# Optimization experiments

Measured on AMD Instinct MI355X. Metric: run time of the kernel, lower is better.

The kernel has to match this reference:

```python
import jax, jax.numpy as jnp
import numpy as np

N = 10000      # nodes
E = 320000     # edges (before self-loops)
IN = 128       # input features
HID = 32       # hidden channels per head
HEADS = 8
OUT = 40       # classes
NEG_SLOPE = 0.2  # PyG GATConv leaky_relu slope


def gat_conv(x, W, a_src, a_dst, b, src, dst, n, concat):
    """One PyG-style GATConv (eval mode, self-loops already in src/dst)."""
    H, C = a_src.shape
    xp = (x @ W).reshape(n, H, C)                       # [N,H,C]
    al_s = jnp.einsum('nhc,hc->nh', xp, a_src)          # [N,H]
    al_d = jnp.einsum('nhc,hc->nh', xp, a_dst)          # [N,H]
    e = jax.nn.leaky_relu(al_s[src] + al_d[dst], NEG_SLOPE)  # [E,H]
    # segment softmax over incoming edges of each dst node
    m = jax.ops.segment_max(e, dst, num_segments=n)
    ee = jnp.exp(e - m[dst])
    s = jax.ops.segment_sum(ee, dst, num_segments=n)
    alpha = ee / (s[dst] + 1e-16)                       # [E,H]
    out = jax.ops.segment_sum(alpha[:, :, None] * xp[src], dst, num_segments=n)  # [N,H,C]
    out = out.reshape(n, H * C) if concat else out.mean(axis=1)
    return out + b


def setup_inputs() -> dict:
    key = jax.random.key(0)
    ks = jax.random.split(key, 16)
    p = lambda k, shape: (jax.random.normal(k, shape, jnp.float32) * 0.1)
    HC = HEADS * HID
    return {
        'x': jax.random.normal(ks[0], (N, IN), jnp.float32),
        'edge_index': jax.random.randint(ks[1], (2, E), 0, N),
        'W1': p(ks[2], (IN, HC)), 'a_src1': p(ks[3], (HEADS, HID)), 'a_dst1': p(ks[4], (HEADS, HID)), 'b1': jnp.zeros((HC,), jnp.float32),
        'W2': p(ks[5], (HC, HC)), 'a_src2': p(ks[6], (HEADS, HID)), 'a_dst2': p(ks[7], (HEADS, HID)), 'b2': jnp.zeros((HC,), jnp.float32),
        'W3': p(ks[8], (HC, OUT)), 'a_src3': p(ks[9], (1, OUT)), 'a_dst3': p(ks[10], (1, OUT)), 'b3': jnp.zeros((OUT,), jnp.float32),
    }


def reference(x, edge_index, W1, a_src1, a_dst1, b1, W2, a_src2, a_dst2, b2,
              W3, a_src3, a_dst3, b3):
    n = x.shape[0]
    loop = jnp.arange(n, dtype=edge_index.dtype)
    src = jnp.concatenate([edge_index[0], loop])   # PyG add_self_loops=True
    dst = jnp.concatenate([edge_index[1], loop])
    h = jax.nn.elu(gat_conv(x, W1, a_src1, a_dst1, b1, src, dst, n, True))
    h = jax.nn.elu(gat_conv(h, W2, a_src2, a_dst2, b2, src, dst, n, True))
    h = gat_conv(h, W3, a_src3, a_dst3, b3, src, dst, n, False)
    return jax.nn.log_softmax(h, axis=1)
```

## Files before the change

### kernel.cpp

```cpp
#include <hip/hip_runtime.h>
#include <hip/hip_bf16.h>
#include <math.h>


#define DEV_INLINE __device__ __forceinline__

typedef __attribute__((ext_vector_type(8))) short short8;
typedef __attribute__((ext_vector_type(4))) float f32x4;
typedef __attribute__((ext_vector_type(2))) float f32x2;
typedef unsigned short ushort_t;
typedef unsigned int uint_t;
typedef unsigned char uchar_t;

#define ELLW 128

#if defined(__has_builtin)
#if __has_builtin(__builtin_amdgcn_cvt_pk_f32_fp8) && __has_builtin(__builtin_amdgcn_cvt_pk_fp8_f32)
#define FP8_HW 1
#endif
#endif
#ifndef FP8_HW
#define FP8_HW 0
#endif

DEV_INLINE float leaky02(float x) { return x > 0.f ? x : 0.2f * x; }
DEV_INLINE float elu1(float x) { return x > 0.f ? x : expm1f(x); }

DEV_INLINE ushort_t f2bf(float f) {
    uint_t u = __float_as_uint(f);
    u += 0x7FFFu + ((u >> 16) & 1u);
    return (ushort_t)(u >> 16);
}
DEV_INLINE float bf2f(ushort_t u) { return __uint_as_float(((uint_t)u) << 16); }


DEV_INLINE uint_t f2fp8(float v) {
#if FP8_HW
    return __builtin_amdgcn_cvt_pk_fp8_f32(v, v, 0, false) & 0xFFu;
#else
    float a = fabsf(v);
    uint_t s = (__float_as_uint(v) >> 24) & 0x80u;
    if (!(a >= 0.0009765625f)) return s;
    if (a >= 448.f) return s | 0x7Eu;
    if (a < 0.015625f) {
        int m = (int)(a * 512.f + 0.5f);
        if (m >= 8) return s | 0x08u;
        return s | (uint_t)m;
    }
    uint_t ab = __float_as_uint(a);
    uint_t r = ab + 0x0007FFFFu + ((ab >> 20) & 1u);
    uint_t e = (r >> 23) - 127u + 7u;
    uint_t m = (r >> 20) & 7u;
    if (e > 15u || (e == 15u && m == 7u)) return s | 0x7Eu;
    return s | (e << 3) | m;
#endif
}

DEV_INLINE void fp8x8_dec(uint2 w, float* f) {
#if FP8_HW
    f32x2 a0 = __builtin_amdgcn_cvt_pk_f32_fp8((int)w.x, false);
    f32x2 a1 = __builtin_amdgcn_cvt_pk_f32_fp8((int)w.x, true);
    f32x2 a2 = __builtin_amdgcn_cvt_pk_f32_fp8((int)w.y, false);
    f32x2 a3 = __builtin_amdgcn_cvt_pk_f32_fp8((int)w.y, true);
    f[0] = a0.x; f[1] = a0.y; f[2] = a1.x; f[3] = a1.y;
    f[4] = a2.x; f[5] = a2.y; f[6] = a3.x; f[7] = a3.y;
#else
    uint_t b[8] = {w.x & 255u, (w.x >> 8) & 255u, (w.x >> 16) & 255u, w.x >> 24,
                   w.y & 255u, (w.y >> 8) & 255u, (w.y >> 16) & 255u, w.y >> 24};
#pragma unroll
    for (int i = 0; i < 8; ++i) {
        uint_t em = b[i] & 0x7Fu;
        float mag = (em >= 8u) ? __uint_as_float(0x3C000000u + (em << 20))
                               : (float)(int)em * 0.001953125f;
        f[i] = (b[i] & 0x80u) ? -mag : mag;
    }
#endif
}


__global__ void prep_kernel(const float* __restrict__ W1, ushort_t* __restrict__ W1T,
                            const float* __restrict__ W2, ushort_t* __restrict__ W2T,
                            const float* __restrict__ W3, ushort_t* __restrict__ W3T,
                            const float* __restrict__ as1, const float* __restrict__ ad1,
                            const float* __restrict__ as2, const float* __restrict__ ad2,
                            const float* __restrict__ as3, const float* __restrict__ ad3,
                            int* __restrict__ cursor, int n) {
    int i = blockIdx.x * blockDim.x + threadIdx.x;
    if (i < n) { cursor[i] = 0; return; }
    i -= n;
    if (i < 128 * 256) {
        int k = i >> 8, c = i & 255;
        W1T[(size_t)c * 128 + k] = f2bf(W1[i]);
        return;
    }
    i -= 128 * 256;
    if (i < 256 * 256) {
        int k = i >> 8, c = i & 255;
        W2T[(size_t)c * 256 + k] = f2bf(W2[i]);
        return;
    }
    i -= 256 * 256;
    if (i < 256 * 40) {
        int k = i / 40, c = i - k * 40;
        W3T[(size_t)c * 256 + k] = f2bf(W3[i]);
        return;
    }
    i -= 256 * 40;
    if (i < 1024) {
        int h = i >> 7, k = i & 127;
        float acc = 0.f;
#pragma unroll
        for (int c = 0; c < 32; ++c) acc += W1[k * 256 + h * 32 + c] * as1[h * 32 + c];
        W1T[(size_t)(256 + h) * 128 + k] = f2bf(acc);
        return;
    }
    i -= 1024;
    if (i < 1024) {
        int h = i >> 7, k = i & 127;
        float acc = 0.f;
#pragma unroll
        for (int c = 0; c < 32; ++c) acc += W1[k * 256 + h * 32 + c] * ad1[h * 32 + c];
        W1T[(size_t)(264 + h) * 128 + k] = f2bf(acc);
        return;
    }
    i -= 1024;
    if (i < 2048) {
        int h = i >> 8, k = i & 255;
        float acc = 0.f;
#pragma unroll
        for (int c = 0; c < 32; ++c) acc += W2[k * 256 + h * 32 + c] * as2[h * 32 + c];
        W2T[(size_t)(256 + h) * 256 + k] = f2bf(acc);
        return;
    }
    i -= 2048;
    if (i < 2048) {
        int h = i >> 8, k = i & 255;
        float acc = 0.f;
#pragma unroll
        for (int c = 0; c < 32; ++c) acc += W2[k * 256 + h * 32 + c] * ad2[h * 32 + c];
        W2T[(size_t)(264 + h) * 256 + k] = f2bf(acc);
        return;
    }
    i -= 2048;
    if (i < 256) {
        float acc = 0.f;
#pragma unroll
        for (int c = 0; c < 40; ++c) acc += W3[i * 40 + c] * as3[c];
        W3T[(size_t)40 * 256 + i] = f2bf(acc);
        return;
    }
    i -= 256;
    if (i < 256) {
        float acc = 0.f;
#pragma unroll
        for (int c = 0; c < 40; ++c) acc += W3[i * 40 + c] * ad3[c];
        W3T[(size_t)41 * 256 + i] = f2bf(acc);
        return;
    }
}


DEV_INLINE int lds_slot(int r, int c) { return r * 4 + ((c + (r >> 1)) & 3); }

DEV_INLINE void gemm_body(ushort_t* __restrict__ As, ushort_t* __restrict__ Bs,
                          const ushort_t* __restrict__ A, const ushort_t* __restrict__ BT,
                          uchar_t* __restrict__ C8,
                          float* __restrict__ ALS, float* __restrict__ ALD,
                          int M, int NOUT, int NH, int NTOT, int K, int bx, int by) {
    const int tid = threadIdx.x;
    const int wave = tid >> 6, lane = tid & 63;
    const int row0 = by * 64;
    const int col0 = bx * 64;

    const int sr = tid >> 2, sc = tid & 3;
    const int a_row = row0 + sr;
    const int b_row = col0 + sr;

    const int fr = lane & 15;
    const int fc = lane >> 4;

    f32x4 acc0 = {}, acc1 = {}, acc2 = {}, acc3 = {};

    for (int k0 = 0; k0 < K; k0 += 32) {
        short8 av = {}, bv = {};
        if (a_row < M) av = *(const short8*)(A + (size_t)a_row * K + k0 + sc * 8);
        if (b_row < NTOT) bv = *(const short8*)(BT + (size_t)b_row * K + k0 + sc * 8);
        __syncthreads();
        *(short8*)(As + lds_slot(sr, sc) * 8) = av;
        *(short8*)(Bs + lds_slot(sr, sc) * 8) = bv;
        __syncthreads();

        const int arow = wave * 16 + fr;
        short8 afrag = *(const short8*)(As + lds_slot(arow, fc) * 8);
        short8 b0 = *(const short8*)(Bs + lds_slot(0 * 16 + fr, fc) * 8);
        short8 b1 = *(const short8*)(Bs + lds_slot(1 * 16 + fr, fc) * 8);
        short8 b2 = *(const short8*)(Bs + lds_slot(2 * 16 + fr, fc) * 8);
        short8 b3 = *(const short8*)(Bs + lds_slot(3 * 16 + fr, fc) * 8);
        acc0 = __builtin_amdgcn_mfma_f32_16x16x32_bf16(afrag, b0, acc0, 0, 0, 0);
        acc1 = __builtin_amdgcn_mfma_f32_16x16x32_bf16(afrag, b1, acc1, 0, 0, 0);
        acc2 = __builtin_amdgcn_mfma_f32_16x16x32_bf16(afrag, b2, acc2, 0, 0, 0);
        acc3 = __builtin_amdgcn_mfma_f32_16x16x32_bf16(afrag, b3, acc3, 0, 0, 0);
    }
    __syncthreads();

    const int crow = row0 + wave * 16 + (lane >> 4) * 4;
    const int ccol = col0 + (lane & 15);
    f32x4 accs[4] = {acc0, acc1, acc2, acc3};
#pragma unroll
    for (int ct = 0; ct < 4; ++ct) {
        int col = ccol + ct * 16;
#pragma unroll
        for (int j = 0; j < 4; ++j) {
            int row = crow + j;
            if (row >= M) continue;
            float v = accs[ct][j];
            if (col < NOUT) {
                C8[(size_t)row * NOUT + col] = (uchar_t)f2fp8(v);
            } else {
                int cc = col - NOUT;
                if (cc < NH) ALS[(size_t)row * NH + cc] = v;
                else if (cc < 2 * NH) ALD[(size_t)row * NH + (cc - NH)] = v;
            }
        }
    }
}

DEV_INLINE void gemm1_body(ushort_t* __restrict__ As, ushort_t* __restrict__ Bs,
                           const float* __restrict__ X, const ushort_t* __restrict__ BT,
                           uchar_t* __restrict__ C8, float* __restrict__ ALS,
                           float* __restrict__ ALD, int M, int bx, int by) {
    const int tid = threadIdx.x;
    const int wave = tid >> 6, lane = tid & 63;
    const int row0 = by * 64;
    const int col0 = bx * 64;

    const int sr = tid >> 2, sc = tid & 3;
    const int a_row = row0 + sr;
    const int b_row = col0 + sr;

    const int fr = lane & 15;
    const int fc = lane >> 4;

    f32x4 acc0 = {}, acc1 = {}, acc2 = {}, acc3 = {};

    for (int k0 = 0; k0 < 128; k0 += 32) {
        short8 av = {}, bv = {};
        if (a_row < M) {
            const float* xp = X + (size_t)a_row * 128 + k0 + sc * 8;
            float4 f0 = *(const float4*)(xp);
            float4 f1 = *(const float4*)(xp + 4);
            av[0] = (short)f2bf(f0.x); av[1] = (short)f2bf(f0.y);
            av[2] = (short)f2bf(f0.z); av[3] = (short)f2bf(f0.w);
            av[4] = (short)f2bf(f1.x); av[5] = (short)f2bf(f1.y);
            av[6] = (short)f2bf(f1.z); av[7] = (short)f2bf(f1.w);
        }
        if (b_row < 272) bv = *(const short8*)(BT + (size_t)b_row * 128 + k0 + sc * 8);
        __syncthreads();
        *(short8*)(As + lds_slot(sr, sc) * 8) = av;
        *(short8*)(Bs + lds_slot(sr, sc) * 8) = bv;
        __syncthreads();

        const int arow = wave * 16 + fr;
        short8 afrag = *(const short8*)(As + lds_slot(arow, fc) * 8);
        short8 b0 = *(const short8*)(Bs + lds_slot(0 * 16 + fr, fc) * 8);
        short8 b1 = *(const short8*)(Bs + lds_slot(1 * 16 + fr, fc) * 8);
        short8 b2 = *(const short8*)(Bs + lds_slot(2 * 16 + fr, fc) * 8);
        short8 b3 = *(const short8*)(Bs + lds_slot(3 * 16 + fr, fc) * 8);
        acc0 = __builtin_amdgcn_mfma_f32_16x16x32_bf16(afrag, b0, acc0, 0, 0, 0);
        acc1 = __builtin_amdgcn_mfma_f32_16x16x32_bf16(afrag, b1, acc1, 0, 0, 0);
        acc2 = __builtin_amdgcn_mfma_f32_16x16x32_bf16(afrag, b2, acc2, 0, 0, 0);
        acc3 = __builtin_amdgcn_mfma_f32_16x16x32_bf16(afrag, b3, acc3, 0, 0, 0);
    }
    __syncthreads();

    const int crow = row0 + wave * 16 + (lane >> 4) * 4;
    const int ccol = col0 + (lane & 15);
    f32x4 accs[4] = {acc0, acc1, acc2, acc3};
#pragma unroll
    for (int ct = 0; ct < 4; ++ct) {
        int col = ccol + ct * 16;
#pragma unroll
        for (int j = 0; j < 4; ++j) {
            int row = crow + j;
            if (row >= M) continue;
            float v = accs[ct][j];
            if (col < 256) {
                C8[(size_t)row * 256 + col] = (uchar_t)f2fp8(v);
            } else {
                int cc = col - 256;
                if (cc < 8) ALS[(size_t)row * 8 + cc] = v;
                else if (cc < 16) ALD[(size_t)row * 8 + (cc - 8)] = v;
            }
        }
    }
}

__global__ __launch_bounds__(256) void gemm_kernel(const ushort_t* __restrict__ A,
                                                   const ushort_t* __restrict__ BT,
                                                   uchar_t* __restrict__ C8,
                                                   float* __restrict__ ALS,
                                                   float* __restrict__ ALD,
                                                   int M, int NOUT, int NH, int NTOT,
                                                   int K, int gx) {
    __shared__ ushort_t As[64 * 32];
    __shared__ ushort_t Bs[64 * 32];
    gemm_body(As, Bs, A, BT, C8, ALS, ALD, M, NOUT, NH, NTOT, K,
              blockIdx.x % gx, blockIdx.x / gx);
}

__global__ __launch_bounds__(256) void scatter_gemm1_kernel(const int* __restrict__ src,
                                                            const int* __restrict__ dst,
                                                            int* __restrict__ cursor,
                                                            int* __restrict__ ell, int e,
                                                            int svb,
                                                            const float* __restrict__ X,
                                                            const ushort_t* __restrict__ BT,
                                                            uchar_t* __restrict__ C8,
                                                            float* __restrict__ ALS,
                                                            float* __restrict__ ALD,
                                                            int M, int gx) {
    __shared__ ushort_t As[64 * 32];
    __shared__ ushort_t Bs[64 * 32];
    if (blockIdx.x < svb) {
        int i = blockIdx.x * 256 + threadIdx.x;
        if (i < e) {
            int d = dst[i];
            int p = atomicAdd(&cursor[d], 1);
            ell[d * ELLW + p] = src[i];
        }
        return;
    }
    int b = blockIdx.x - svb;
    gemm1_body(As, Bs, X, BT, C8, ALS, ALD, M, b % gx, b / gx);
}


template <int FUSE3>
__global__ __launch_bounds__(256) void aggregate_h8_kernel(const uchar_t* __restrict__ xp8,
                                                           const float* __restrict__ als,
                                                           const float* __restrict__ ald,
                                                           const int* __restrict__ degv,
                                                           const int* __restrict__ ell,
                                                           const float* __restrict__ bias,
                                                           ushort_t* __restrict__ out,
                                                           const ushort_t* __restrict__ W3T,
                                                           ushort_t* __restrict__ xp3,
                                                           float* __restrict__ als3,
                                                           float* __restrict__ ald3,
                                                           int n) {
    int node = (blockIdx.x * blockDim.x + threadIdx.x) >> 6;
    int lane = threadIdx.x & 63;
    if (node >= n) return;
    const int half = lane >> 5;
    const int lh = lane & 31;
    const int ch = lh * 8;
    const int head = lh >> 2;
    const int deg = degv[node];
    const int rs = node * ELLW, re = rs + deg;
    const float ad = ald[node * 8 + head];
    const float m = leaky02(als[node * 8 + head] + ad);

    float acc[8];
    float ssum;
    if (half == 0) {
        uint2 sv = *(const uint2*)(xp8 + (size_t)node * 256 + ch);
        float sf[8];
        fp8x8_dec(sv, sf);
#pragma unroll
        for (int i = 0; i < 8; ++i) acc[i] = sf[i];
        ssum = 1.0f;
    } else {
#pragma unroll
        for (int i = 0; i < 8; ++i) acc[i] = 0.f;
        ssum = 0.f;
    }

    for (int base = rs; base < re; base += 64) {
        const int cnt = (re - base < 64) ? (re - base) : 64;
        int myi = (lane < cnt) ? ell[base + lane] : 0;
        int j = 0;
        for (; j + 8 <= cnt; j += 8) {
            int s0 = __shfl(myi, j + half);
            int s1 = __shfl(myi, j + 2 + half);
            int s2 = __shfl(myi, j + 4 + half);
            int s3 = __shfl(myi, j + 6 + half);
            float a0 = als[s0 * 8 + head];
            float a1 = als[s1 * 8 + head];
            float a2 = als[s2 * 8 + head];
            float a3 = als[s3 * 8 + head];
            uint2 v0 = *(const uint2*)(xp8 + (size_t)s0 * 256 + ch);
            uint2 v1 = *(const uint2*)(xp8 + (size_t)s1 * 256 + ch);
            uint2 v2 = *(const uint2*)(xp8 + (size_t)s2 * 256 + ch);
            uint2 v3 = *(const uint2*)(xp8 + (size_t)s3 * 256 + ch);
            float p0 = __expf(leaky02(a0 + ad) - m);
            float p1 = __expf(leaky02(a1 + ad) - m);
            float p2 = __expf(leaky02(a2 + ad) - m);
            float p3 = __expf(leaky02(a3 + ad) - m);
            ssum += (p0 + p1) + (p2 + p3);
            float f0[8], f1[8], f2[8], f3[8];
            fp8x8_dec(v0, f0);
            fp8x8_dec(v1, f1);
            fp8x8_dec(v2, f2);
            fp8x8_dec(v3, f3);
#pragma unroll
            for (int i = 0; i < 8; ++i)
                acc[i] += (p0 * f0[i] + p1 * f1[i]) + (p2 * f2[i] + p3 * f3[i]);
        }
        for (; j < cnt; j += 2) {
            int jj = j + half;
            int s = __shfl(myi, jj & 63);
            bool valid = jj < cnt;
            float a = als[s * 8 + head];
            uint2 v = *(const uint2*)(xp8 + (size_t)s * 256 + ch);
            float p = valid ? __expf(leaky02(a + ad) - m) : 0.f;
            ssum += p;
            float fv[8];
            fp8x8_dec(v, fv);
#pragma unroll
            for (int i = 0; i < 8; ++i) acc[i] += p * fv[i];
        }
    }

    ssum += __shfl_xor(ssum, 32);
#pragma unroll
    for (int i = 0; i < 8; ++i) acc[i] += __shfl_xor(acc[i], 32);

    if (FUSE3 == 0) {
        if (half == 0) {
            float inv = 1.f / ssum;
            float4 ba = *(const float4*)(bias + ch);
            float4 bb = *(const float4*)(bias + ch + 4);
            float bv[8] = {ba.x, ba.y, ba.z, ba.w, bb.x, bb.y, bb.z, bb.w};
            short8 o;
#pragma unroll
            for (int i = 0; i < 8; ++i) o[i] = (short)f2bf(elu1(acc[i] * inv + bv[i]));
            *(short8*)(out + (size_t)node * 256 + ch) = o;
        }
    } else {
        float inv = 1.f / ssum;
        float4 ba = *(const float4*)(bias + ch);
        float4 bb = *(const float4*)(bias + ch + 4);
        float bv[8] = {ba.x, ba.y, ba.z, ba.w, bb.x, bb.y, bb.z, bb.w};
        float hf[8];
#pragma unroll
        for (int i = 0; i < 8; ++i) hf[i] = elu1(acc[i] * inv + bv[i]);

        float res = 0.f;
#pragma unroll
        for (int idx = 0; idx < 21; ++idx) {
            int c = half * 21 + idx;
            short8 w = *(const short8*)(W3T + (size_t)c * 256 + ch);
            float p = hf[0] * bf2f((ushort_t)w[0]) + hf[1] * bf2f((ushort_t)w[1])
                    + hf[2] * bf2f((ushort_t)w[2]) + hf[3] * bf2f((ushort_t)w[3])
                    + hf[4] * bf2f((ushort_t)w[4]) + hf[5] * bf2f((ushort_t)w[5])
                    + hf[6] * bf2f((ushort_t)w[6]) + hf[7] * bf2f((ushort_t)w[7]);
            p += __shfl_xor(p, 1);
            p += __shfl_xor(p, 2);
            p += __shfl_xor(p, 4);
            p += __shfl_xor(p, 8);
            p += __shfl_xor(p, 16);
            if (lh == idx) res = p;
        }
        if (lh < 21) {
            int c = half * 21 + lh;
            if (c < 40)      xp3[(size_t)node * 40 + c] = f2bf(res);
            else if (c == 40) als3[node] = res;
            else             ald3[node] = res;
        }
    }
}


__global__ __launch_bounds__(256) void aggregate_out_kernel(const ushort_t* __restrict__ xp,
                                                            const float* __restrict__ als,
                                                            const float* __restrict__ ald,
                                                            const int* __restrict__ degv,
                                                            const int* __restrict__ ell,
                                                            const float* __restrict__ bias,
                                                            float* __restrict__ out, int n) {
    int node = (blockIdx.x * blockDim.x + threadIdx.x) >> 6;
    int lane = threadIdx.x & 63;
    if (node >= n) return;
    const int half = lane >> 5;
    const int lh = lane & 31;
    const bool act = lh < 20;
    const int ch = lh * 2;
    const int deg = degv[node];
    const int rs = node * ELLW, re = rs + deg;
    const float ad = ald[node];
    const float m = leaky02(als[node] + ad);

    float a0, a1, ssum;
    if (half == 0) {
        if (act) {
            ushort2 sv = *(const ushort2*)(xp + (size_t)node * 40 + ch);
            a0 = bf2f(sv.x); a1 = bf2f(sv.y);
        } else { a0 = a1 = 0.f; }
        ssum = 1.0f;
    } else { a0 = a1 = 0.f; ssum = 0.f; }

    for (int base = rs; base < re; base += 64) {
        const int cnt = (re - base < 64) ? (re - base) : 64;
        int myi = (lane < cnt) ? ell[base + lane] : 0;
        int j = 0;
        for (; j + 8 <= cnt; j += 8) {
            int s0 = __shfl(myi, j + half);
            int s1 = __shfl(myi, j + 2 + half);
            int s2 = __shfl(myi, j + 4 + half);
            int s3 = __shfl(myi, j + 6 + half);
            float e0 = als[s0];
            float e1 = als[s1];
            float e2 = als[s2];
            float e3 = als[s3];
            ushort2 v0 = act ? *(const ushort2*)(xp + (size_t)s0 * 40 + ch) : ushort2{0, 0};
            ushort2 v1 = act ? *(const ushort2*)(xp + (size_t)s1 * 40 + ch) : ushort2{0, 0};
            ushort2 v2 = act ? *(const ushort2*)(xp + (size_t)s2 * 40 + ch) : ushort2{0, 0};
            ushort2 v3 = act ? *(const ushort2*)(xp + (size_t)s3 * 40 + ch) : ushort2{0, 0};
            float p0 = __expf(leaky02(e0 + ad) - m);
            float p1 = __expf(leaky02(e1 + ad) - m);
            float p2 = __expf(leaky02(e2 + ad) - m);
            float p3 = __expf(leaky02(e3 + ad) - m);
            ssum += (p0 + p1) + (p2 + p3);
            a0 += (p0 * bf2f(v0.x) + p1 * bf2f(v1.x)) + (p2 * bf2f(v2.x) + p3 * bf2f(v3.x));
            a1 += (p0 * bf2f(v0.y) + p1 * bf2f(v1.y)) + (p2 * bf2f(v2.y) + p3 * bf2f(v3.y));
        }
        for (; j < cnt; j += 2) {
            int jj = j + half;
            int s = __shfl(myi, jj & 63);
            bool valid = jj < cnt;
            float a = als[s];
            ushort2 v = act ? *(const ushort2*)(xp + (size_t)s * 40 + ch) : ushort2{0, 0};
            float p = valid ? __expf(leaky02(a + ad) - m) : 0.f;
            ssum += p;
            a0 += p * bf2f(v.x);
            a1 += p * bf2f(v.y);
        }
    }

    ssum += __shfl_xor(ssum, 32);
    a0 += __shfl_xor(a0, 32);
    a1 += __shfl_xor(a1, 32);

    float inv = 1.f / ssum;
    float2 b2 = act ? *(const float2*)(bias + ch) : float2{0.f, 0.f};
    float o0 = act ? (a0 * inv + b2.x) : -INFINITY;
    float o1 = act ? (a1 * inv + b2.y) : -INFINITY;

    float mx = fmaxf(o0, o1);
#pragma unroll
    for (int off = 16; off >= 1; off >>= 1) mx = fmaxf(mx, __shfl_xor(mx, off));
    float ex = act ? (__expf(o0 - mx) + __expf(o1 - mx)) : 0.f;
#pragma unroll
    for (int off = 16; off >= 1; off >>= 1) ex += __shfl_xor(ex, off);
    float lse = mx + __logf(ex);
    if (half == 0 && act) {
        float2 o = {o0 - lse, o1 - lse};
        *(float2*)(out + (size_t)node * 40 + ch) = o;
    }
}


extern "C" void kernel_launch(void* const* d_in, const int* in_sizes, int n_in,
                              void* d_out, int out_size, void* d_ws, size_t ws_size,
                              hipStream_t stream) {
    const float* x      = (const float*)d_in[0];
    const int*   edge   = (const int*)d_in[1];
    const float* W1     = (const float*)d_in[2];
    const float* a_src1 = (const float*)d_in[3];
    const float* a_dst1 = (const float*)d_in[4];
    const float* b1     = (const float*)d_in[5];
    const float* W2     = (const float*)d_in[6];
    const float* a_src2 = (const float*)d_in[7];
    const float* a_dst2 = (const float*)d_in[8];
    const float* b2     = (const float*)d_in[9];
    const float* W3     = (const float*)d_in[10];
    const float* a_src3 = (const float*)d_in[11];
    const float* a_dst3 = (const float*)d_in[12];
    const float* b3     = (const float*)d_in[13];
    float* out = (float*)d_out;

    const int n = in_sizes[0] / 128;
    const int e = in_sizes[1] / 2;

    char* ws = (char*)d_ws;
    size_t off = 0;
    auto alloc = [&](size_t bytes) -> void* {
        void* p = ws + off;
        off += (bytes + 255) & ~(size_t)255;
        return p;
    };
    uchar_t*  xp8       = (uchar_t*)alloc((size_t)n * 256);
    ushort_t* h_bf      = (ushort_t*)alloc((size_t)n * 256 * 2);
    ushort_t* xp3       = (ushort_t*)alloc((size_t)n * 40 * 2);
    ushort_t* W1T       = (ushort_t*)alloc((size_t)272 * 128 * 2);
    ushort_t* W2T       = (ushort_t*)alloc((size_t)272 * 256 * 2);
    ushort_t* W3T       = (ushort_t*)alloc((size_t)42 * 256 * 2);
    float*    als       = (float*)alloc((size_t)n * 8 * 4);
    float*    ald       = (float*)alloc((size_t)n * 8 * 4);
    float*    als3      = (float*)alloc((size_t)n * 4);
    float*    ald3      = (float*)alloc((size_t)n * 4);
    int*      cursor    = (int*)alloc((size_t)n * 4);
    int*      ell       = (int*)alloc((size_t)n * ELLW * 4);
    (void)ws_size;

    const int* srcs = edge;
    const int* dsts = edge + e;

    const int mby = (n + 63) / 64;
    const int svb = (e + 255) / 256;

    {
        int prep_total = n + 128 * 256 + 256 * 256 + 256 * 40
                       + 1024 + 1024 + 2048 + 2048 + 256 + 256;
        prep_kernel<<<(prep_total + 255) / 256, 256, 0, stream>>>(
            W1, W1T, W2, W2T, W3, W3T,
            a_src1, a_dst1, a_src2, a_dst2, a_src3, a_dst3, cursor, n);
    }
    scatter_gemm1_kernel<<<svb + 5 * mby, 256, 0, stream>>>(
        srcs, dsts, cursor, ell, e, svb, x, W1T, xp8, als, ald, n, 5);

    const int agg_grid = (n * 64 + 255) / 256;

    aggregate_h8_kernel<0><<<agg_grid, 256, 0, stream>>>(
        xp8, als, ald, cursor, ell, b1, h_bf, nullptr, nullptr, nullptr, nullptr, n);
    gemm_kernel<<<5 * mby, 256, 0, stream>>>(h_bf, W2T, xp8, als, ald,
                                             n, 256, 8, 272, 256, 5);
    aggregate_h8_kernel<1><<<agg_grid, 256, 0, stream>>>(
        xp8, als, ald, cursor, ell, b2, nullptr, W3T, xp3, als3, ald3, n);
    aggregate_out_kernel<<<agg_grid, 256, 0, stream>>>(xp3, als3, ald3, cursor, ell, b3, out, n);
}
```

Before: 101.5 us.

## Fuse attention logits into GEMM epilogue and fold weight prep into scatter kernel

```diff
diff --git a/kernel.cpp b/kernel.cpp
--- a/kernel.cpp
+++ b/kernel.cpp
@@ -78,22 +78,10 @@
 }
 
 
-__global__ void prep_kernel(const float* __restrict__ W1, ushort_t* __restrict__ W1T,
-                            const float* __restrict__ W2, ushort_t* __restrict__ W2T,
-                            const float* __restrict__ W3, ushort_t* __restrict__ W3T,
-                            const float* __restrict__ as1, const float* __restrict__ ad1,
-                            const float* __restrict__ as2, const float* __restrict__ ad2,
-                            const float* __restrict__ as3, const float* __restrict__ ad3,
-                            int* __restrict__ cursor, int n) {
-    int i = blockIdx.x * blockDim.x + threadIdx.x;
-    if (i < n) { cursor[i] = 0; return; }
-    i -= n;
-    if (i < 128 * 256) {
-        int k = i >> 8, c = i & 255;
-        W1T[(size_t)c * 128 + k] = f2bf(W1[i]);
-        return;
-    }
-    i -= 128 * 256;
+DEV_INLINE void prep_body(int i,
+                          const float* __restrict__ W2, ushort_t* __restrict__ W2T,
+                          const float* __restrict__ W3, ushort_t* __restrict__ W3T,
+                          const float* __restrict__ as3, const float* __restrict__ ad3) {
     if (i < 256 * 256) {
         int k = i >> 8, c = i & 255;
         W2T[(size_t)c * 256 + k] = f2bf(W2[i]);
@@ -106,42 +94,6 @@
         return;
     }
     i -= 256 * 40;
-    if (i < 1024) {
-        int h = i >> 7, k = i & 127;
-        float acc = 0.f;
-#pragma unroll
-        for (int c = 0; c < 32; ++c) acc += W1[k * 256 + h * 32 + c] * as1[h * 32 + c];
-        W1T[(size_t)(256 + h) * 128 + k] = f2bf(acc);
-        return;
-    }
-    i -= 1024;
-    if (i < 1024) {
-        int h = i >> 7, k = i & 127;
-        float acc = 0.f;
-#pragma unroll
-        for (int c = 0; c < 32; ++c) acc += W1[k * 256 + h * 32 + c] * ad1[h * 32 + c];
-        W1T[(size_t)(264 + h) * 128 + k] = f2bf(acc);
-        return;
-    }
-    i -= 1024;
-    if (i < 2048) {
-        int h = i >> 8, k = i & 255;
-        float acc = 0.f;
-#pragma unroll
-        for (int c = 0; c < 32; ++c) acc += W2[k * 256 + h * 32 + c] * as2[h * 32 + c];
-        W2T[(size_t)(256 + h) * 256 + k] = f2bf(acc);
-        return;
-    }
-    i -= 2048;
-    if (i < 2048) {
-        int h = i >> 8, k = i & 255;
-        float acc = 0.f;
-#pragma unroll
-        for (int c = 0; c < 32; ++c) acc += W2[k * 256 + h * 32 + c] * ad2[h * 32 + c];
-        W2T[(size_t)(264 + h) * 256 + k] = f2bf(acc);
-        return;
-    }
-    i -= 2048;
     if (i < 256) {
         float acc = 0.f;
 #pragma unroll
@@ -160,13 +112,48 @@
 }
 
 
+DEV_INLINE void epilogue_al(const f32x4* accs, const float* __restrict__ AS,
+                            const float* __restrict__ AD, float* __restrict__ ALS,
+                            float* __restrict__ ALD, int M, int col0, int crow,
+                            int lane, int bx) {
+    const int lc = lane & 15;
+    float as[4], ad[4];
+#pragma unroll
+    for (int ct = 0; ct < 4; ++ct) {
+        as[ct] = AS[col0 + lc + ct * 16];
+        ad[ct] = AD[col0 + lc + ct * 16];
+    }
+#pragma unroll
+    for (int j = 0; j < 4; ++j) {
+        float s0 = accs[0][j] * as[0] + accs[1][j] * as[1];
+        float s1 = accs[2][j] * as[2] + accs[3][j] * as[3];
+        float d0 = accs[0][j] * ad[0] + accs[1][j] * ad[1];
+        float d1 = accs[2][j] * ad[2] + accs[3][j] * ad[3];
+#pragma unroll
+        for (int off = 1; off < 16; off <<= 1) {
+            s0 += __shfl_xor(s0, off);
+            s1 += __shfl_xor(s1, off);
+            d0 += __shfl_xor(d0, off);
+            d1 += __shfl_xor(d1, off);
+        }
+        int row = crow + j;
+        if (lc == 0 && row < M) {
+            ALS[(size_t)row * 8 + 2 * bx]     = s0;
+            ALS[(size_t)row * 8 + 2 * bx + 1] = s1;
+            ALD[(size_t)row * 8 + 2 * bx]     = d0;
+            ALD[(size_t)row * 8 + 2 * bx + 1] = d1;
+        }
+    }
+}
+
+
 DEV_INLINE int lds_slot(int r, int c) { return r * 4 + ((c + (r >> 1)) & 3); }
 
-DEV_INLINE void gemm_body(ushort_t* __restrict__ As, ushort_t* __restrict__ Bs,
-                          const ushort_t* __restrict__ A, const ushort_t* __restrict__ BT,
-                          uchar_t* __restrict__ C8,
-                          float* __restrict__ ALS, float* __restrict__ ALD,
-                          int M, int NOUT, int NH, int NTOT, int K, int bx, int by) {
+DEV_INLINE void gemm2_body(ushort_t* __restrict__ As, ushort_t* __restrict__ Bs,
+                           const ushort_t* __restrict__ A, const ushort_t* __restrict__ BT,
+                           uchar_t* __restrict__ C8, const float* __restrict__ AS,
+                           const float* __restrict__ AD, float* __restrict__ ALS,
+                           float* __restrict__ ALD, int M, int bx, int by) {
     const int tid = threadIdx.x;
     const int wave = tid >> 6, lane = tid & 63;
     const int row0 = by * 64;
@@ -181,10 +168,10 @@
 
     f32x4 acc0 = {}, acc1 = {}, acc2 = {}, acc3 = {};
 
-    for (int k0 = 0; k0 < K; k0 += 32) {
-        short8 av = {}, bv = {};
-        if (a_row < M) av = *(const short8*)(A + (size_t)a_row * K + k0 + sc * 8);
-        if (b_row < NTOT) bv = *(const short8*)(BT + (size_t)b_row * K + k0 + sc * 8);
+    for (int k0 = 0; k0 < 256; k0 += 32) {
+        short8 av = {}, bv;
+        if (a_row < M) av = *(const short8*)(A + (size_t)a_row * 256 + k0 + sc * 8);
+        bv = *(const short8*)(BT + (size_t)b_row * 256 + k0 + sc * 8);
         __syncthreads();
         *(short8*)(As + lds_slot(sr, sc) * 8) = av;
         *(short8*)(Bs + lds_slot(sr, sc) * 8) = bv;
@@ -212,22 +199,16 @@
 #pragma unroll
         for (int j = 0; j < 4; ++j) {
             int row = crow + j;
-            if (row >= M) continue;
-            float v = accs[ct][j];
-            if (col < NOUT) {
-                C8[(size_t)row * NOUT + col] = (uchar_t)f2fp8(v);
-            } else {
-                int cc = col - NOUT;
-                if (cc < NH) ALS[(size_t)row * NH + cc] = v;
-                else if (cc < 2 * NH) ALD[(size_t)row * NH + (cc - NH)] = v;
-            }
-        }
-    }
+            if (row < M) C8[(size_t)row * 256 + col] = (uchar_t)f2fp8(accs[ct][j]);
+        }
+    }
+    epilogue_al(accs, AS, AD, ALS, ALD, M, col0, crow, lane, bx);
 }
 
 DEV_INLINE void gemm1_body(ushort_t* __restrict__ As, ushort_t* __restrict__ Bs,
-                           const float* __restrict__ X, const ushort_t* __restrict__ BT,
-                           uchar_t* __restrict__ C8, float* __restrict__ ALS,
+                           const float* __restrict__ X, const float* __restrict__ W1,
+                           uchar_t* __restrict__ C8, const float* __restrict__ AS,
+                           const float* __restrict__ AD, float* __restrict__ ALS,
                            float* __restrict__ ALD, int M, int bx, int by) {
     const int tid = threadIdx.x;
     const int wave = tid >> 6, lane = tid & 63;
@@ -244,7 +225,7 @@
     f32x4 acc0 = {}, acc1 = {}, acc2 = {}, acc3 = {};
 
     for (int k0 = 0; k0 < 128; k0 += 32) {
-        short8 av = {}, bv = {};
+        short8 av = {}, bv;
         if (a_row < M) {
             const float* xp = X + (size_t)a_row * 128 + k0 + sc * 8;
             float4 f0 = *(const float4*)(xp);
@@ -254,7 +235,9 @@
             av[4] = (short)f2bf(f1.x); av[5] = (short)f2bf(f1.y);
             av[6] = (short)f2bf(f1.z); av[7] = (short)f2bf(f1.w);
         }
-        if (b_row < 272) bv = *(const short8*)(BT + (size_t)b_row * 128 + k0 + sc * 8);
+#pragma unroll
+        for (int t = 0; t < 8; ++t)
+            bv[t] = (short)f2bf(W1[(size_t)(k0 + sc * 8 + t) * 256 + b_row]);
         __syncthreads();
         *(short8*)(As + lds_slot(sr, sc) * 8) = av;
         *(short8*)(Bs + lds_slot(sr, sc) * 8) = bv;
@@ -282,43 +265,41 @@
 #pragma unroll
         for (int j = 0; j < 4; ++j) {
             int row = crow + j;
-            if (row >= M) continue;
-            float v = accs[ct][j];
-            if (col < 256) {
-                C8[(size_t)row * 256 + col] = (uchar_t)f2fp8(v);
-            } else {
-                int cc = col - 256;
-                if (cc < 8) ALS[(size_t)row * 8 + cc] = v;
-                else if (cc < 16) ALD[(size_t)row * 8 + (cc - 8)] = v;
-            }
-        }
-    }
-}
-
-__global__ __launch_bounds__(256) void gemm_kernel(const ushort_t* __restrict__ A,
-                                                   const ushort_t* __restrict__ BT,
-                                                   uchar_t* __restrict__ C8,
-                                                   float* __restrict__ ALS,
-                                                   float* __restrict__ ALD,
-                                                   int M, int NOUT, int NH, int NTOT,
-                                                   int K, int gx) {
+            if (row < M) C8[(size_t)row * 256 + col] = (uchar_t)f2fp8(accs[ct][j]);
+        }
+    }
+    epilogue_al(accs, AS, AD, ALS, ALD, M, col0, crow, lane, bx);
+}
+
+__global__ __launch_bounds__(256) void gemm2_kernel(const ushort_t* __restrict__ A,
+                                                    const ushort_t* __restrict__ BT,
+                                                    uchar_t* __restrict__ C8,
+                                                    const float* __restrict__ AS,
+                                                    const float* __restrict__ AD,
+                                                    float* __restrict__ ALS,
+                                                    float* __restrict__ ALD, int M) {
     __shared__ ushort_t As[64 * 32];
     __shared__ ushort_t Bs[64 * 32];
-    gemm_body(As, Bs, A, BT, C8, ALS, ALD, M, NOUT, NH, NTOT, K,
-              blockIdx.x % gx, blockIdx.x / gx);
-}
-
-__global__ __launch_bounds__(256) void scatter_gemm1_kernel(const int* __restrict__ src,
-                                                            const int* __restrict__ dst,
-                                                            int* __restrict__ cursor,
-                                                            int* __restrict__ ell, int e,
-                                                            int svb,
-                                                            const float* __restrict__ X,
-                                                            const ushort_t* __restrict__ BT,
-                                                            uchar_t* __restrict__ C8,
-                                                            float* __restrict__ ALS,
-                                                            float* __restrict__ ALD,
-                                                            int M, int gx) {
+    gemm2_body(As, Bs, A, BT, C8, AS, AD, ALS, ALD, M, blockIdx.x & 3, blockIdx.x >> 2);
+}
+
+__global__ __launch_bounds__(256) void k2_kernel(const int* __restrict__ src,
+                                                 const int* __restrict__ dst,
+                                                 int* __restrict__ cursor,
+                                                 int* __restrict__ ell, int e, int svb,
+                                                 const float* __restrict__ X,
+                                                 const float* __restrict__ W1,
+                                                 uchar_t* __restrict__ C8,
+                                                 const float* __restrict__ AS,
+                                                 const float* __restrict__ AD,
+                                                 float* __restrict__ ALS,
+                                                 float* __restrict__ ALD, int M, int gvb,
+                                                 const float* __restrict__ W2,
+                                                 ushort_t* __restrict__ W2T,
+                                                 const float* __restrict__ W3,
+                                                 ushort_t* __restrict__ W3T,
+                                                 const float* __restrict__ as3,
+                                                 const float* __restrict__ ad3) {
     __shared__ ushort_t As[64 * 32];
     __shared__ ushort_t Bs[64 * 32];
     if (blockIdx.x < svb) {
@@ -331,7 +312,11 @@
         return;
     }
     int b = blockIdx.x - svb;
-    gemm1_body(As, Bs, X, BT, C8, ALS, ALD, M, b % gx, b / gx);
+    if (b < gvb) {
+        gemm1_body(As, Bs, X, W1, C8, AS, AD, ALS, ALD, M, b & 3, b >> 2);
+        return;
+    }
+    prep_body((b - gvb) * 256 + threadIdx.x, W2, W2T, W3, W3T, as3, ad3);
 }
 
 
@@ -463,9 +448,9 @@
         }
         if (lh < 21) {
             int c = half * 21 + lh;
-            if (c < 40)      xp3[(size_t)node * 40 + c] = f2bf(res);
+            if (c < 40)       xp3[(size_t)node * 40 + c] = f2bf(res);
             else if (c == 40) als3[node] = res;
-            else             ald3[node] = res;
+            else              ald3[node] = res;
         }
     }
 }
@@ -592,8 +577,7 @@
     uchar_t*  xp8       = (uchar_t*)alloc((size_t)n * 256);
     ushort_t* h_bf      = (ushort_t*)alloc((size_t)n * 256 * 2);
     ushort_t* xp3       = (ushort_t*)alloc((size_t)n * 40 * 2);
-    ushort_t* W1T       = (ushort_t*)alloc((size_t)272 * 128 * 2);
-    ushort_t* W2T       = (ushort_t*)alloc((size_t)272 * 256 * 2);
+    ushort_t* W2T       = (ushort_t*)alloc((size_t)256 * 256 * 2);
     ushort_t* W3T       = (ushort_t*)alloc((size_t)42 * 256 * 2);
     float*    als       = (float*)alloc((size_t)n * 8 * 4);
     float*    ald       = (float*)alloc((size_t)n * 8 * 4);
@@ -608,23 +592,20 @@
 
     const int mby = (n + 63) / 64;
     const int svb = (e + 255) / 256;
-
-    {
-        int prep_total = n + 128 * 256 + 256 * 256 + 256 * 40
-                       + 1024 + 1024 + 2048 + 2048 + 256 + 256;
-        prep_kernel<<<(prep_total + 255) / 256, 256, 0, stream>>>(
-            W1, W1T, W2, W2T, W3, W3T,
-            a_src1, a_dst1, a_src2, a_dst2, a_src3, a_dst3, cursor, n);
-    }
-    scatter_gemm1_kernel<<<svb + 5 * mby, 256, 0, stream>>>(
-        srcs, dsts, cursor, ell, e, svb, x, W1T, xp8, als, ald, n, 5);
+    const int gvb = 4 * mby;
+    const int pvb = (256 * 256 + 256 * 40 + 512 + 255) / 256;
+
+    hipMemsetAsync(cursor, 0, (size_t)n * 4, stream);
+    k2_kernel<<<svb + gvb + pvb, 256, 0, stream>>>(
+        srcs, dsts, cursor, ell, e, svb,
+        x, W1, xp8, a_src1, a_dst1, als, ald, n, gvb,
+        W2, W2T, W3, W3T, a_src3, a_dst3);
 
     const int agg_grid = (n * 64 + 255) / 256;
 
     aggregate_h8_kernel<0><<<agg_grid, 256, 0, stream>>>(
         xp8, als, ald, cursor, ell, b1, h_bf, nullptr, nullptr, nullptr, nullptr, n);
-    gemm_kernel<<<5 * mby, 256, 0, stream>>>(h_bf, W2T, xp8, als, ald,
-                                             n, 256, 8, 272, 256, 5);
+    gemm2_kernel<<<4 * mby, 256, 0, stream>>>(h_bf, W2T, xp8, a_src2, a_dst2, als, ald, n);
     aggregate_h8_kernel<1><<<agg_grid, 256, 0, stream>>>(
         xp8, als, ald, cursor, ell, b2, nullptr, W3T, xp3, als3, ald3, n);
     aggregate_out_kernel<<<agg_grid, 256, 0, stream>>>(xp3, als3, ald3, cursor, ell, b3, out, n);
```

Result: slower. 106.0 us (+4.5%).
